# Kernel optimization log

Hardware: AMD Instinct MI355X
Metric: run time of the kernel (lower is better)

## Reference

```python
import jax, jax.numpy as jnp
import numpy as np

DIM = 512
NUM_HEADS = 8
HEAD_DIM = DIM // NUM_HEADS
SCALE = HEAD_DIM ** -0.5


def setup_inputs() -> dict:
    key = jax.random.key(0)
    ks = jax.random.split(key, 5)
    B, N = 4, 2048
    x = jax.random.normal(ks[0], (B, N, DIM), dtype=jnp.float32)
    # Learned parameters (torch nn.Linear style: y = x @ W.T + b)
    w_qkv = jax.random.normal(ks[1], (3 * DIM, DIM), dtype=jnp.float32) * (DIM ** -0.5)
    b_qkv = jnp.zeros((3 * DIM,), dtype=jnp.float32)
    w_proj = jax.random.normal(ks[2], (DIM, DIM), dtype=jnp.float32) * (DIM ** -0.5)
    b_proj = jnp.zeros((DIM,), dtype=jnp.float32)
    return {"x": x, "w_qkv": w_qkv, "b_qkv": b_qkv, "w_proj": w_proj, "b_proj": b_proj}


def reference(x, w_qkv, b_qkv, w_proj, b_proj):
    B, N, C = x.shape
    qkv = x @ w_qkv.T + b_qkv                      # [B, N, 3C]
    qkv = qkv.reshape(B, N, 3, NUM_HEADS, HEAD_DIM)
    qkv = jnp.transpose(qkv, (2, 0, 3, 1, 4))      # [3, B, H, N, d]
    q, k, v = qkv[0], qkv[1], qkv[2]
    attn = jnp.einsum("bhqd,bhkd->bhqk", q, k) * SCALE  # [B, H, N, N]
    attn = jax.nn.softmax(attn, axis=-1)
    out = jnp.einsum("bhqk,bhkd->bhqd", attn, v)   # [B, H, N, d]
    out = jnp.transpose(out, (0, 2, 1, 3)).reshape(B, N, C)
    return out @ w_proj.T + b_proj
```

## Files before the change

kernel.cpp:

```cpp
#include <hip/hip_runtime.h>

#define DIM 512
#define NHEAD 8
#define HDIM 64
#define BATCH 4
#define SEQ 2048
#define MTOT (BATCH*SEQ)
#define SCALE 0.125f
#define LOG2E 1.4426950408889634f

typedef __bf16 bf16_t;
typedef __bf16 bf16x8 __attribute__((ext_vector_type(8)));
typedef __bf16 bf16x4 __attribute__((ext_vector_type(4)));
typedef float f32x4 __attribute__((ext_vector_type(4)));

__global__ __launch_bounds__(256) void cvt_kernel(const float* __restrict__ in,
                                                  bf16_t* __restrict__ out) {
    int i = (blockIdx.x * 256 + threadIdx.x) * 4;
    float4 v = *reinterpret_cast<const float4*>(in + i);
    bf16x4 o;
    o[0] = (bf16_t)v.x; o[1] = (bf16_t)v.y; o[2] = (bf16_t)v.z; o[3] = (bf16_t)v.w;
    *reinterpret_cast<bf16x4*>(out + i) = o;
}

__global__ __launch_bounds__(256) void gemm_qkv_kernel(
    const bf16_t* __restrict__ X, const bf16_t* __restrict__ W,
    const float* __restrict__ bias,
    bf16_t* __restrict__ Qo, bf16_t* __restrict__ Ko, bf16_t* __restrict__ Vto)
{
    __shared__ bf16_t As[128][72];
    __shared__ bf16_t Bs[128][72];
    const int tid = threadIdx.x;
    const int wave = tid >> 6, lane = tid & 63;
    const int lhi = lane >> 4, llo = lane & 15;
    const int o = blockIdx.x;
    const int x = o & 7, i0 = o >> 3;
    const int m0 = (x * 8 + (i0 & 7)) * 128;
    const int n0 = (i0 >> 3) * 128;
    const int wr = (wave >> 1) * 64, wc = (wave & 1) * 64;
    f32x4 acc[4][4] = {};

    for (int k0 = 0; k0 < DIM; k0 += 64) {
        #pragma unroll
        for (int p = 0; p < 4; ++p) {
            int c = p * 256 + tid;
            int r = c >> 3, cc = (c & 7) * 8;
            *reinterpret_cast<uint4*>(&As[r][cc]) =
                *reinterpret_cast<const uint4*>(X + (size_t)(m0 + r) * DIM + k0 + cc);
            *reinterpret_cast<uint4*>(&Bs[r][cc]) =
                *reinterpret_cast<const uint4*>(W + (size_t)(n0 + r) * DIM + k0 + cc);
        }
        __syncthreads();
        #pragma unroll
        for (int ks = 0; ks < 2; ++ks) {
            bf16x8 af[4], bfr[4];
            #pragma unroll
            for (int i = 0; i < 4; ++i)
                af[i] = *reinterpret_cast<const bf16x8*>(&As[wr + i*16 + llo][ks*32 + lhi*8]);
            #pragma unroll
            for (int j = 0; j < 4; ++j)
                bfr[j] = *reinterpret_cast<const bf16x8*>(&Bs[wc + j*16 + llo][ks*32 + lhi*8]);
            #pragma unroll
            for (int i = 0; i < 4; ++i)
                #pragma unroll
                for (int j = 0; j < 4; ++j)
                    acc[i][j] = __builtin_amdgcn_mfma_f32_16x16x32_bf16(af[i], bfr[j], acc[i][j], 0, 0, 0);
        }
        __syncthreads();
    }

    #pragma unroll
    for (int j = 0; j < 4; ++j) {
        int col = n0 + wc + j*16 + llo;
        int which = col >> 9;
        int hh = (col >> 6) & 7;
        int dd = col & 63;
        float bv = bias[col];
        #pragma unroll
        for (int i = 0; i < 4; ++i) {
            #pragma unroll
            for (int r = 0; r < 4; ++r) {
                int m = m0 + wr + i*16 + lhi*4 + r;
                int b = m >> 11, ns = m & 2047;
                float v = acc[i][j][r] + bv;
                size_t bh = (size_t)(b * NHEAD + hh);
                if (which == 0)
                    Qo[(bh * SEQ + ns) * HDIM + dd] = (bf16_t)(v * (SCALE * LOG2E));
                else if (which == 1)
                    Ko[(bh * SEQ + ns) * HDIM + dd] = (bf16_t)v;
                else
                    Vto[(bh * HDIM + dd) * SEQ + ns] = (bf16_t)v;
            }
        }
    }
}

__global__ __launch_bounds__(512) void attn_kernel(
    const bf16_t* __restrict__ Q, const bf16_t* __restrict__ K,
    const bf16_t* __restrict__ Vt, bf16_t* __restrict__ O)
{
    __shared__ bf16_t Ks[2][64][72];
    __shared__ bf16_t Vs[2][64][72];
    const int tid = threadIdx.x;
    const int wave = tid >> 6, lane = tid & 63;
    const int lhi = lane >> 4, llo = lane & 15;
    const int o = blockIdx.x;
    const int w = (o & 7) * 32 + (o >> 3);
    const int qt = w & 7, bh = w >> 3;
    const bf16_t* Qb = Q + (size_t)bh * SEQ * HDIM;
    const bf16_t* Kb = K + (size_t)bh * SEQ * HDIM;
    const bf16_t* Vb = Vt + (size_t)bh * HDIM * SEQ;
    const int q0 = qt * 256 + wave * 32;

    const int sr = tid >> 3;
    const int scc = (tid & 7) * 8;

    bf16x8 aq[2][2];
    #pragma unroll
    for (int qb = 0; qb < 2; ++qb)
        #pragma unroll
        for (int ks = 0; ks < 2; ++ks)
            aq[qb][ks] = *reinterpret_cast<const bf16x8*>(
                Qb + (size_t)(q0 + qb*16 + llo) * HDIM + ks*32 + lhi*8);

    f32x4 acc_o[2][4] = {};
    float mstat[2], lstat[2];
    mstat[0] = mstat[1] = -1e30f;
    lstat[0] = lstat[1] = 0.f;
    const float THR = 8.0f * LOG2E;

    uint4 kreg, vreg;
    kreg = *reinterpret_cast<const uint4*>(Kb + (size_t)sr * HDIM + scc);
    vreg = *reinterpret_cast<const uint4*>(Vb + (size_t)sr * SEQ + scc);
    *reinterpret_cast<uint4*>(&Ks[0][sr][scc]) = kreg;
    *reinterpret_cast<uint4*>(&Vs[0][sr][scc]) = vreg;
    __syncthreads();

    const int NT = SEQ / 64;
    for (int kt = 0; kt < NT; ++kt) {
        const int cur = kt & 1, nxt = cur ^ 1;

        if (kt + 1 < NT) {
            kreg = *reinterpret_cast<const uint4*>(
                Kb + (size_t)((kt+1)*64 + sr) * HDIM + scc);
            vreg = *reinterpret_cast<const uint4*>(
                Vb + (size_t)sr * SEQ + (kt+1)*64 + scc);
        }

        f32x4 s[2][4] = {};
        #pragma unroll
        for (int kb = 0; kb < 4; ++kb) {
            #pragma unroll
            for (int ks = 0; ks < 2; ++ks) {
                bf16x8 kf = *reinterpret_cast<const bf16x8*>(&Ks[cur][kb*16 + llo][ks*32 + lhi*8]);
                #pragma unroll
                for (int qb = 0; qb < 2; ++qb)
                    s[qb][kb] = __builtin_amdgcn_mfma_f32_16x16x32_bf16(kf, aq[qb][ks], s[qb][kb], 0, 0, 0);
            }
        }

        float lmax[2];
        bool ok = true;
        #pragma unroll
        for (int qb = 0; qb < 2; ++qb) {
            float mx = s[qb][0][0];
            #pragma unroll
            for (int kb = 0; kb < 4; ++kb)
                #pragma unroll
                for (int r = 0; r < 4; ++r) mx = fmaxf(mx, s[qb][kb][r]);
            lmax[qb] = mx;
            ok &= (mx <= mstat[qb] + THR);
        }

        if (!__all(ok)) {
            #pragma unroll
            for (int qb = 0; qb < 2; ++qb) {
                float mx = lmax[qb];
                mx = fmaxf(mx, __shfl_xor(mx, 16, 64));
                mx = fmaxf(mx, __shfl_xor(mx, 32, 64));
                float mold = mstat[qb];
                float mn = fmaxf(mold, mx);
                float alpha = __builtin_amdgcn_exp2f(mold - mn);
                mstat[qb] = mn;
                lstat[qb] *= alpha;
                #pragma unroll
                for (int r = 0; r < 4; ++r) {
                    float av = __shfl(alpha, (lane & 48) >> 2 | r, 64);
                    #pragma unroll
                    for (int db = 0; db < 4; ++db) acc_o[qb][db][r] *= av;
                }
            }
        }

        #pragma unroll
        for (int qb = 0; qb < 2; ++qb) {
            float rs = 0.f;
            #pragma unroll
            for (int kb = 0; kb < 4; ++kb)
                #pragma unroll
                for (int r = 0; r < 4; ++r) {
                    float pv = __builtin_amdgcn_exp2f(s[qb][kb][r] - mstat[qb]);
                    s[qb][kb][r] = pv;
                    rs += pv;
                }
            rs += __shfl_xor(rs, 16, 64);
            rs += __shfl_xor(rs, 32, 64);
            lstat[qb] += rs;
        }

        bf16x8 ap[2][2];
        #pragma unroll
        for (int qb = 0; qb < 2; ++qb)
            #pragma unroll
            for (int kp = 0; kp < 2; ++kp)
                #pragma unroll
                for (int j = 0; j < 4; ++j) {
                    ap[qb][kp][j]     = (bf16_t)s[qb][2*kp][j];
                    ap[qb][kp][4 + j] = (bf16_t)s[qb][2*kp + 1][j];
                }

        #pragma unroll
        for (int kp = 0; kp < 2; ++kp) {
            #pragma unroll
            for (int db = 0; db < 4; ++db) {
                bf16x4 l0 = *reinterpret_cast<const bf16x4*>(&Vs[cur][db*16 + llo][(2*kp)*16 + lhi*4]);
                bf16x4 l1 = *reinterpret_cast<const bf16x4*>(&Vs[cur][db*16 + llo][(2*kp+1)*16 + lhi*4]);
                bf16x8 bv;
                #pragma unroll
                for (int j = 0; j < 4; ++j) { bv[j] = l0[j]; bv[4 + j] = l1[j]; }
                #pragma unroll
                for (int qb = 0; qb < 2; ++qb)
                    acc_o[qb][db] = __builtin_amdgcn_mfma_f32_16x16x32_bf16(ap[qb][kp], bv, acc_o[qb][db], 0, 0, 0);
            }
        }

        if (kt + 1 < NT) {
            *reinterpret_cast<uint4*>(&Ks[nxt][sr][scc]) = kreg;
            *reinterpret_cast<uint4*>(&Vs[nxt][sr][scc]) = vreg;
        }
        __syncthreads();
    }

    const int b = bh >> 3, h = bh & 7;
    #pragma unroll
    for (int qb = 0; qb < 2; ++qb) {
        float inv = 1.0f / lstat[qb];
        #pragma unroll
        for (int r = 0; r < 4; ++r) {
            float iv = __shfl(inv, (lane & 48) >> 2 | r, 64);
            int q = q0 + qb*16 + lhi*4 + r;
            #pragma unroll
            for (int db = 0; db < 4; ++db)
                O[(size_t)(b * SEQ + q) * DIM + h*HDIM + db*16 + llo] =
                    (bf16_t)(acc_o[qb][db][r] * iv);
        }
    }
}

__global__ __launch_bounds__(256) void gemm_proj_kernel(
    const bf16_t* __restrict__ X, const bf16_t* __restrict__ W,
    const float* __restrict__ bias, float* __restrict__ out)
{
    __shared__ bf16_t As[128][72];
    __shared__ bf16_t Bs[128][72];
    const int tid = threadIdx.x;
    const int wave = tid >> 6, lane = tid & 63;
    const int lhi = lane >> 4, llo = lane & 15;
    const int o = blockIdx.x;
    const int x = o & 7, i0 = o >> 3;
    const int m0 = (x * 8 + (i0 & 7)) * 128;
    const int n0 = (i0 >> 3) * 128;
    const int wr = (wave >> 1) * 64, wc = (wave & 1) * 64;
    f32x4 acc[4][4] = {};

    for (int k0 = 0; k0 < DIM; k0 += 64) {
        #pragma unroll
        for (int p = 0; p < 4; ++p) {
            int c = p * 256 + tid;
            int r = c >> 3, cc = (c & 7) * 8;
            *reinterpret_cast<uint4*>(&As[r][cc]) =
                *reinterpret_cast<const uint4*>(X + (size_t)(m0 + r) * DIM + k0 + cc);
            *reinterpret_cast<uint4*>(&Bs[r][cc]) =
                *reinterpret_cast<const uint4*>(W + (size_t)(n0 + r) * DIM + k0 + cc);
        }
        __syncthreads();
        #pragma unroll
        for (int ks = 0; ks < 2; ++ks) {
            bf16x8 af[4], bfr[4];
            #pragma unroll
            for (int i = 0; i < 4; ++i)
                af[i] = *reinterpret_cast<const bf16x8*>(&As[wr + i*16 + llo][ks*32 + lhi*8]);
            #pragma unroll
            for (int j = 0; j < 4; ++j)
                bfr[j] = *reinterpret_cast<const bf16x8*>(&Bs[wc + j*16 + llo][ks*32 + lhi*8]);
            #pragma unroll
            for (int i = 0; i < 4; ++i)
                #pragma unroll
                for (int j = 0; j < 4; ++j)
                    acc[i][j] = __builtin_amdgcn_mfma_f32_16x16x32_bf16(af[i], bfr[j], acc[i][j], 0, 0, 0);
        }
        __syncthreads();
    }

    #pragma unroll
    for (int j = 0; j < 4; ++j) {
        int col = n0 + wc + j*16 + llo;
        float bv = bias[col];
        #pragma unroll
        for (int i = 0; i < 4; ++i)
            #pragma unroll
            for (int r = 0; r < 4; ++r) {
                int m = m0 + wr + i*16 + lhi*4 + r;
                out[(size_t)m * DIM + col] = acc[i][j][r] + bv;
            }
    }
}

extern "C" void kernel_launch(void* const* d_in, const int* in_sizes, int n_in,
                              void* d_out, int out_size, void* d_ws, size_t ws_size,
                              hipStream_t stream) {
    const float* x      = (const float*)d_in[0];
    const float* w_qkv  = (const float*)d_in[1];
    const float* b_qkv  = (const float*)d_in[2];
    const float* w_proj = (const float*)d_in[3];
    const float* b_proj = (const float*)d_in[4];
    float* out = (float*)d_out;

    const size_t NX  = (size_t)MTOT * DIM;
    const size_t NWQ = (size_t)3 * DIM * DIM;
    const size_t NWP = (size_t)DIM * DIM;
    const size_t NQ  = (size_t)BATCH * NHEAD * SEQ * HDIM;

    bf16_t* Xb    = (bf16_t*)d_ws;
    bf16_t* Wqkv  = Xb + NX;
    bf16_t* Wproj = Wqkv + NWQ;
    bf16_t* Qb    = Wproj + NWP;
    bf16_t* Kb    = Qb + NQ;
    bf16_t* Vtb   = Kb + NQ;
    bf16_t* AOb   = Vtb + NQ;

    cvt_kernel<<<(int)(NX  / 1024), 256, 0, stream>>>(x, Xb);
    cvt_kernel<<<(int)(NWQ / 1024), 256, 0, stream>>>(w_qkv, Wqkv);
    cvt_kernel<<<(int)(NWP / 1024), 256, 0, stream>>>(w_proj, Wproj);

    gemm_qkv_kernel<<<768, 256, 0, stream>>>(Xb, Wqkv, b_qkv, Qb, Kb, Vtb);

    attn_kernel<<<256, 512, 0, stream>>>(Qb, Kb, Vtb, AOb);

    gemm_proj_kernel<<<256, 256, 0, stream>>>(AOb, Wproj, b_proj, out);
}
```

Before: 103.5 us.

## Use async global-to-LDS copies in GEMMs and widen attention KV tiles

Both GEMM kernels now stage tiles with global_load_lds direct-to-LDS copies instead of register round trips, dropping the LDS padding, and raise wave priority around MFMA blocks. The attention kernel doubles the KV tile to 128 keys and pre-permutes V in shared memory so each lane reads one contiguous bf16x8 fragment. It also interleaves the exp/pack step with the PV MFMAs per 32-key chunk. The unpadded GEMM LDS layout risks bank conflicts, and the async copy has no explicit vmcnt wait before the barrier, which may race.

```diff
diff --git a/kernel.cpp b/kernel.cpp
--- a/kernel.cpp
+++ b/kernel.cpp
@@ -14,6 +14,10 @@
 typedef __bf16 bf16x4 __attribute__((ext_vector_type(4)));
 typedef float f32x4 __attribute__((ext_vector_type(4)));
 
+#define ASYNC_COPY16(g, l) __builtin_amdgcn_global_load_lds( \
+    (const __attribute__((address_space(1))) void*)(g),      \
+    (__attribute__((address_space(3))) void*)(l), 16, 0, 0)
+
 __global__ __launch_bounds__(256) void cvt_kernel(const float* __restrict__ in,
                                                   bf16_t* __restrict__ out) {
     int i = (blockIdx.x * 256 + threadIdx.x) * 4;
@@ -28,8 +32,8 @@
     const float* __restrict__ bias,
     bf16_t* __restrict__ Qo, bf16_t* __restrict__ Ko, bf16_t* __restrict__ Vto)
 {
-    __shared__ bf16_t As[128][72];
-    __shared__ bf16_t Bs[128][72];
+    __shared__ bf16_t As[128][64];
+    __shared__ bf16_t Bs[128][64];
     const int tid = threadIdx.x;
     const int wave = tid >> 6, lane = tid & 63;
     const int lhi = lane >> 4, llo = lane & 15;
@@ -40,15 +44,16 @@
     const int wr = (wave >> 1) * 64, wc = (wave & 1) * 64;
     f32x4 acc[4][4] = {};
 
+    const int srow = wave * 32 + (lane >> 3);
+    const int scol = (lane & 7) * 8;
+    const bf16_t* gA = X + (size_t)(m0 + srow) * DIM + scol;
+    const bf16_t* gB = W + (size_t)(n0 + srow) * DIM + scol;
+
     for (int k0 = 0; k0 < DIM; k0 += 64) {
         #pragma unroll
         for (int p = 0; p < 4; ++p) {
-            int c = p * 256 + tid;
-            int r = c >> 3, cc = (c & 7) * 8;
-            *reinterpret_cast<uint4*>(&As[r][cc]) =
-                *reinterpret_cast<const uint4*>(X + (size_t)(m0 + r) * DIM + k0 + cc);
-            *reinterpret_cast<uint4*>(&Bs[r][cc]) =
-                *reinterpret_cast<const uint4*>(W + (size_t)(n0 + r) * DIM + k0 + cc);
+            ASYNC_COPY16(gA + (size_t)p * 8 * DIM + k0, &As[wave*32 + p*8][0]);
+            ASYNC_COPY16(gB + (size_t)p * 8 * DIM + k0, &Bs[wave*32 + p*8][0]);
         }
         __syncthreads();
         #pragma unroll
@@ -60,11 +65,13 @@
             #pragma unroll
             for (int j = 0; j < 4; ++j)
                 bfr[j] = *reinterpret_cast<const bf16x8*>(&Bs[wc + j*16 + llo][ks*32 + lhi*8]);
+            __builtin_amdgcn_s_setprio(1);
             #pragma unroll
             for (int i = 0; i < 4; ++i)
                 #pragma unroll
                 for (int j = 0; j < 4; ++j)
                     acc[i][j] = __builtin_amdgcn_mfma_f32_16x16x32_bf16(af[i], bfr[j], acc[i][j], 0, 0, 0);
+            __builtin_amdgcn_s_setprio(0);
         }
         __syncthreads();
     }
@@ -99,8 +106,8 @@
     const bf16_t* __restrict__ Q, const bf16_t* __restrict__ K,
     const bf16_t* __restrict__ Vt, bf16_t* __restrict__ O)
 {
-    __shared__ bf16_t Ks[2][64][72];
-    __shared__ bf16_t Vs[2][64][72];
+    __shared__ bf16_t Ks[2][128][72];
+    __shared__ bf16_t Vs[2][64][136];
     const int tid = threadIdx.x;
     const int wave = tid >> 6, lane = tid & 63;
     const int lhi = lane >> 4, llo = lane & 15;
@@ -112,8 +119,12 @@
     const bf16_t* Vb = Vt + (size_t)bh * HDIM * SEQ;
     const int q0 = qt * 256 + wave * 32;
 
-    const int sr = tid >> 3;
-    const int scc = (tid & 7) * 8;
+    const int ksr = tid >> 3, kscc = (tid & 7) * 8;
+    const int vd0 = tid >> 4, vg0 = tid & 15;
+    const int vd1 = (tid + 512) >> 4;
+    auto pk_first  = [](int g) { return 32*(g>>2) + 8*((2*g)&3)   + 4*((g>>1)&1); };
+    auto pk_second = [](int g) { return 32*(g>>2) + 8*((2*g+1)&3) + 4*((g>>1)&1); };
+    const int pkA = pk_first(vg0), pkB = pk_second(vg0);
 
     bf16x8 aq[2][2];
     #pragma unroll
@@ -129,27 +140,39 @@
     lstat[0] = lstat[1] = 0.f;
     const float THR = 8.0f * LOG2E;
 
-    uint4 kreg, vreg;
-    kreg = *reinterpret_cast<const uint4*>(Kb + (size_t)sr * HDIM + scc);
-    vreg = *reinterpret_cast<const uint4*>(Vb + (size_t)sr * SEQ + scc);
-    *reinterpret_cast<uint4*>(&Ks[0][sr][scc]) = kreg;
-    *reinterpret_cast<uint4*>(&Vs[0][sr][scc]) = vreg;
+    uint4 kreg[2], vreg[2];
+    kreg[0] = *reinterpret_cast<const uint4*>(Kb + (size_t)ksr * HDIM + kscc);
+    kreg[1] = *reinterpret_cast<const uint4*>(Kb + (size_t)(ksr + 64) * HDIM + kscc);
+    vreg[0] = *reinterpret_cast<const uint4*>(Vb + (size_t)vd0 * SEQ + vg0*8);
+    vreg[1] = *reinterpret_cast<const uint4*>(Vb + (size_t)vd1 * SEQ + vg0*8);
+    *reinterpret_cast<uint4*>(&Ks[0][ksr][kscc]) = kreg[0];
+    *reinterpret_cast<uint4*>(&Ks[0][ksr + 64][kscc]) = kreg[1];
+    *reinterpret_cast<uint2*>(&Vs[0][vd0][pkA]) = make_uint2(vreg[0].x, vreg[0].y);
+    *reinterpret_cast<uint2*>(&Vs[0][vd0][pkB]) = make_uint2(vreg[0].z, vreg[0].w);
+    *reinterpret_cast<uint2*>(&Vs[0][vd1][pkA]) = make_uint2(vreg[1].x, vreg[1].y);
+    *reinterpret_cast<uint2*>(&Vs[0][vd1][pkB]) = make_uint2(vreg[1].z, vreg[1].w);
     __syncthreads();
 
-    const int NT = SEQ / 64;
+    const int NT = SEQ / 128;
     for (int kt = 0; kt < NT; ++kt) {
         const int cur = kt & 1, nxt = cur ^ 1;
 
         if (kt + 1 < NT) {
-            kreg = *reinterpret_cast<const uint4*>(
-                Kb + (size_t)((kt+1)*64 + sr) * HDIM + scc);
-            vreg = *reinterpret_cast<const uint4*>(
-                Vb + (size_t)sr * SEQ + (kt+1)*64 + scc);
-        }
-
-        f32x4 s[2][4] = {};
-        #pragma unroll
-        for (int kb = 0; kb < 4; ++kb) {
+            const size_t koff = (size_t)(kt + 1) * 128;
+            kreg[0] = *reinterpret_cast<const uint4*>(Kb + (koff + ksr) * HDIM + kscc);
+            kreg[1] = *reinterpret_cast<const uint4*>(Kb + (koff + ksr + 64) * HDIM + kscc);
+            vreg[0] = *reinterpret_cast<const uint4*>(Vb + (size_t)vd0 * SEQ + koff + vg0*8);
+            vreg[1] = *reinterpret_cast<const uint4*>(Vb + (size_t)vd1 * SEQ + koff + vg0*8);
+        }
+
+        f32x4 s[2][8];
+        #pragma unroll
+        for (int qb = 0; qb < 2; ++qb)
+            #pragma unroll
+            for (int kb = 0; kb < 8; ++kb) s[qb][kb] = f32x4{0.f, 0.f, 0.f, 0.f};
+        __builtin_amdgcn_s_setprio(1);
+        #pragma unroll
+        for (int kb = 0; kb < 8; ++kb) {
             #pragma unroll
             for (int ks = 0; ks < 2; ++ks) {
                 bf16x8 kf = *reinterpret_cast<const bf16x8*>(&Ks[cur][kb*16 + llo][ks*32 + lhi*8]);
@@ -158,6 +181,7 @@
                     s[qb][kb] = __builtin_amdgcn_mfma_f32_16x16x32_bf16(kf, aq[qb][ks], s[qb][kb], 0, 0, 0);
             }
         }
+        __builtin_amdgcn_s_setprio(0);
 
         float lmax[2];
         bool ok = true;
@@ -165,7 +189,7 @@
         for (int qb = 0; qb < 2; ++qb) {
             float mx = s[qb][0][0];
             #pragma unroll
-            for (int kb = 0; kb < 4; ++kb)
+            for (int kb = 0; kb < 8; ++kb)
                 #pragma unroll
                 for (int r = 0; r < 4; ++r) mx = fmaxf(mx, s[qb][kb][r]);
             lmax[qb] = mx;
@@ -192,51 +216,46 @@
             }
         }
 
+        float rs[2] = {0.f, 0.f};
+        #pragma unroll
+        for (int kp = 0; kp < 4; ++kp) {
+            bf16x8 ap[2];
+            #pragma unroll
+            for (int qb = 0; qb < 2; ++qb) {
+                #pragma unroll
+                for (int j = 0; j < 4; ++j) {
+                    float p0 = __builtin_amdgcn_exp2f(s[qb][2*kp][j]     - mstat[qb]);
+                    float p1 = __builtin_amdgcn_exp2f(s[qb][2*kp + 1][j] - mstat[qb]);
+                    rs[qb] += p0 + p1;
+                    ap[qb][j]     = (bf16_t)p0;
+                    ap[qb][4 + j] = (bf16_t)p1;
+                }
+            }
+            __builtin_amdgcn_s_setprio(1);
+            #pragma unroll
+            for (int db = 0; db < 4; ++db) {
+                bf16x8 bv = *reinterpret_cast<const bf16x8*>(&Vs[cur][db*16 + llo][kp*32 + lhi*8]);
+                #pragma unroll
+                for (int qb = 0; qb < 2; ++qb)
+                    acc_o[qb][db] = __builtin_amdgcn_mfma_f32_16x16x32_bf16(ap[qb], bv, acc_o[qb][db], 0, 0, 0);
+            }
+            __builtin_amdgcn_s_setprio(0);
+        }
         #pragma unroll
         for (int qb = 0; qb < 2; ++qb) {
-            float rs = 0.f;
-            #pragma unroll
-            for (int kb = 0; kb < 4; ++kb)
-                #pragma unroll
-                for (int r = 0; r < 4; ++r) {
-                    float pv = __builtin_amdgcn_exp2f(s[qb][kb][r] - mstat[qb]);
-                    s[qb][kb][r] = pv;
-                    rs += pv;
-                }
-            rs += __shfl_xor(rs, 16, 64);
-            rs += __shfl_xor(rs, 32, 64);
-            lstat[qb] += rs;
-        }
-
-        bf16x8 ap[2][2];
-        #pragma unroll
-        for (int qb = 0; qb < 2; ++qb)
-            #pragma unroll
-            for (int kp = 0; kp < 2; ++kp)
-                #pragma unroll
-                for (int j = 0; j < 4; ++j) {
-                    ap[qb][kp][j]     = (bf16_t)s[qb][2*kp][j];
-                    ap[qb][kp][4 + j] = (bf16_t)s[qb][2*kp + 1][j];
-                }
-
-        #pragma unroll
-        for (int kp = 0; kp < 2; ++kp) {
-            #pragma unroll
-            for (int db = 0; db < 4; ++db) {
-                bf16x4 l0 = *reinterpret_cast<const bf16x4*>(&Vs[cur][db*16 + llo][(2*kp)*16 + lhi*4]);
-                bf16x4 l1 = *reinterpret_cast<const bf16x4*>(&Vs[cur][db*16 + llo][(2*kp+1)*16 + lhi*4]);
-                bf16x8 bv;
-                #pragma unroll
-                for (int j = 0; j < 4; ++j) { bv[j] = l0[j]; bv[4 + j] = l1[j]; }
-                #pragma unroll
-                for (int qb = 0; qb < 2; ++qb)
-                    acc_o[qb][db] = __builtin_amdgcn_mfma_f32_16x16x32_bf16(ap[qb][kp], bv, acc_o[qb][db], 0, 0, 0);
-            }
+            float r = rs[qb];
+            r += __shfl_xor(r, 16, 64);
+            r += __shfl_xor(r, 32, 64);
+            lstat[qb] += r;
         }
 
         if (kt + 1 < NT) {
-            *reinterpret_cast<uint4*>(&Ks[nxt][sr][scc]) = kreg;
-            *reinterpret_cast<uint4*>(&Vs[nxt][sr][scc]) = vreg;
+            *reinterpret_cast<uint4*>(&Ks[nxt][ksr][kscc]) = kreg[0];
+            *reinterpret_cast<uint4*>(&Ks[nxt][ksr + 64][kscc]) = kreg[1];
+            *reinterpret_cast<uint2*>(&Vs[nxt][vd0][pkA]) = make_uint2(vreg[0].x, vreg[0].y);
+            *reinterpret_cast<uint2*>(&Vs[nxt][vd0][pkB]) = make_uint2(vreg[0].z, vreg[0].w);
+            *reinterpret_cast<uint2*>(&Vs[nxt][vd1][pkA]) = make_uint2(vreg[1].x, vreg[1].y);
+            *reinterpret_cast<uint2*>(&Vs[nxt][vd1][pkB]) = make_uint2(vreg[1].z, vreg[1].w);
         }
         __syncthreads();
     }
@@ -261,8 +280,8 @@
     const bf16_t* __restrict__ X, const bf16_t* __restrict__ W,
     const float* __restrict__ bias, float* __restrict__ out)
 {
-    __shared__ bf16_t As[128][72];
-    __shared__ bf16_t Bs[128][72];
+    __shared__ bf16_t As[128][64];
+    __shared__ bf16_t Bs[128][64];
     const int tid = threadIdx.x;
     const int wave = tid >> 6, lane = tid & 63;
     const int lhi = lane >> 4, llo = lane & 15;
@@ -273,15 +292,16 @@
     const int wr = (wave >> 1) * 64, wc = (wave & 1) * 64;
     f32x4 acc[4][4] = {};
 
+    const int srow = wave * 32 + (lane >> 3);
+    const int scol = (lane & 7) * 8;
+    const bf16_t* gA = X + (size_t)(m0 + srow) * DIM + scol;
+    const bf16_t* gB = W + (size_t)(n0 + srow) * DIM + scol;
+
     for (int k0 = 0; k0 < DIM; k0 += 64) {
         #pragma unroll
         for (int p = 0; p < 4; ++p) {
-            int c = p * 256 + tid;
-            int r = c >> 3, cc = (c & 7) * 8;
-            *reinterpret_cast<uint4*>(&As[r][cc]) =
-                *reinterpret_cast<const uint4*>(X + (size_t)(m0 + r) * DIM + k0 + cc);
-            *reinterpret_cast<uint4*>(&Bs[r][cc]) =
-                *reinterpret_cast<const uint4*>(W + (size_t)(n0 + r) * DIM + k0 + cc);
+            ASYNC_COPY16(gA + (size_t)p * 8 * DIM + k0, &As[wave*32 + p*8][0]);
+            ASYNC_COPY16(gB + (size_t)p * 8 * DIM + k0, &Bs[wave*32 + p*8][0]);
         }
         __syncthreads();
         #pragma unroll
@@ -293,11 +313,13 @@
             #pragma unroll
             for (int j = 0; j < 4; ++j)
                 bfr[j] = *reinterpret_cast<const bf16x8*>(&Bs[wc + j*16 + llo][ks*32 + lhi*8]);
+            __builtin_amdgcn_s_setprio(1);
             #pragma unroll
             for (int i = 0; i < 4; ++i)
                 #pragma unroll
                 for (int j = 0; j < 4; ++j)
                     acc[i][j] = __builtin_amdgcn_mfma_f32_16x16x32_bf16(af[i], bfr[j], acc[i][j], 0, 0, 0);
+            __builtin_amdgcn_s_setprio(0);
         }
         __syncthreads();
     }
```

Result: no change. 101.9 us (-1.5%).
